# Performance work log

Measured on AMD Instinct MI355X. Metric: run time of the kernel, lower is better.

The kernel has to match this reference:

```python
import jax, jax.numpy as jnp
import numpy as np

N, E, D, H, G, L, EF = 50000, 800000, 128, 256, 512, 3, 8
BN_EPS = 1e-5


def _bn(h, g, b):
    # torch BatchNorm1d in training mode: biased batch stats over the node axis
    m = h.mean(0)
    v = h.var(0)
    return g * (h - m) * jax.lax.rsqrt(v + BN_EPS) + b


def setup_inputs() -> dict:
    ks = jax.random.split(jax.random.key(0), 12)
    sc = 0.05
    return {
        "x": jax.random.normal(ks[0], (N, D), jnp.float32),
        "edge_attr": jax.random.normal(ks[1], (E, EF), jnp.float32),
        "vn_emb": jnp.zeros((1, D), jnp.float32),  # init.constant_(0)
        "We": jax.random.normal(ks[2], (L, EF, D)) * sc,
        "be": jnp.zeros((L, D)),
        "W1": jax.random.normal(ks[3], (L, D, H)) * sc,
        "b1": jnp.zeros((L, H)),
        "g1": jnp.ones((L, H)),
        "bt1": jnp.zeros((L, H)),
        "W2": jax.random.normal(ks[4], (L, H, D)) * sc,
        "b2": jnp.zeros((L, D)),
        "gb": jnp.ones((L, D)),
        "bb": jnp.zeros((L, D)),
        "Wv1": jax.random.normal(ks[5], (L - 1, D, H)) * sc,
        "bv1": jnp.zeros((L - 1, H)),
        "gv1": jnp.ones((L - 1, H)),
        "btv1": jnp.zeros((L - 1, H)),
        "Wv2": jax.random.normal(ks[6], (L - 1, H, D)) * sc,
        "bv2": jnp.zeros((L - 1, D)),
        "gv2": jnp.ones((L - 1, D)),
        "btv2": jnp.zeros((L - 1, D)),
        "edge_index": jax.random.randint(ks[7], (2, E), 0, N),
        "batch": jnp.sort(jax.random.randint(ks[8], (N,), 0, G)),
    }


def reference(x, edge_attr, vn_emb, We, be, W1, b1, g1, bt1, W2, b2, gb, bb,
              Wv1, bv1, gv1, btv1, Wv2, bv2, gv2, btv2, edge_index, batch):
    src, dst = edge_index[0], edge_index[1]
    vn = jnp.broadcast_to(vn_emb, (G, D))  # Embedding(1, D) looked up for every graph
    h = x  # node_encoder is None -> encoded_node = x
    for l in range(L):
        h_in = h + vn[batch]                              # virtual-node broadcast (gather)
        e = edge_attr @ We[l] + be[l]                     # per-layer edge encoder
        msg = jax.nn.relu(h_in[src] + e)                  # GIN message, [E, D]
        aggr = jax.ops.segment_sum(msg, dst, num_segments=N)
        z = h_in + aggr                                   # (1+eps)*h + aggr, eps=0
        z = jax.nn.relu(_bn(z @ W1[l] + b1[l], g1[l], bt1[l]))
        h = _bn(z @ W2[l] + b2[l], gb[l], bb[l])          # conv MLP out + outer BatchNorm
        if l < L - 1:
            h = jax.nn.relu(h)                            # dropout ratio 0 -> identity
            pooled = jax.ops.segment_sum(h_in, batch, num_segments=G) + vn
            t = jax.nn.relu(_bn(pooled @ Wv1[l] + bv1[l], gv1[l], btv1[l]))
            vn = jax.nn.relu(_bn(t @ Wv2[l] + bv2[l], gv2[l], btv2[l]))
    return h  # JK == 'last'
```

## Files before the change

kernel.cpp:

```cpp
#include <hip/hip_runtime.h>
#include <hip/hip_bf16.h>

#define N_NODES 50000
#define N_EDGES 800000
#define DIM 128
#define HID 256
#define N_GRAPH 512
#define N_LAYER 3
#define EFEAT 8
#define BN_EPS 1e-5f
#define MAX_GROUPS 240000
#define AGGR_WAVES 8192

typedef unsigned short u16;
typedef unsigned int u32;

using bf16x8_t = short __attribute__((ext_vector_type(8)));
using f32x4_t  = float __attribute__((ext_vector_type(4)));
using f32x2    = float __attribute__((ext_vector_type(2)));
using f32x4v   = float __attribute__((ext_vector_type(4)));


__device__ __forceinline__ void atomic_add_f(float* p, float v) {
    unsafeAtomicAdd(p, v);
}
__device__ __forceinline__ u16 f2bf(float x) {
    union { float f; u32 u; } v; v.f = x;
    u32 r = v.u + 0x7FFF + ((v.u >> 16) & 1);
    return (u16)(r >> 16);
}
__device__ __forceinline__ float bf2f(u16 u) {
    union { u32 i; float f; } v; v.i = (u32)u << 16; return v.f;
}
__device__ __forceinline__ float2 up2(u32 p) {
    return make_float2(bf2f((u16)(p & 0xFFFF)), bf2f((u16)(p >> 16)));
}
__device__ __forceinline__ u32 pk2(float a, float b) {
    return (u32)f2bf(a) | ((u32)f2bf(b) << 16);
}
__device__ __forceinline__ f32x2 up2p(u32 p) {
    union { u32 u[2]; f32x2 f; } v;
    v.u[0] = p << 16;
    v.u[1] = p & 0xFFFF0000u;
    return v.f;
}
__device__ __forceinline__ f32x2 splat2(float x) {
    f32x2 r; r.x = x; r.y = x; return r;
}

__global__ __launch_bounds__(256) void wconv_kernel(
    const float* __restrict__ W1, const float* __restrict__ W2,
    u16* __restrict__ W1t, u16* __restrict__ W2t)
{
    int idx = blockIdx.x * 256 + threadIdx.x;
    if (idx >= 6 * 32768) return;
    int m = idx >> 15;
    int off = idx & 32767;
    int l = m >> 1;
    if ((m & 1) == 0) {
        int r = off >> 8, c = off & 255;
        W1t[(size_t)l * 32768 + c * 128 + r] = f2bf(W1[(size_t)l * 32768 + r * 256 + c]);
    } else {
        int r = off >> 7, c = off & 127;
        W2t[(size_t)l * 32768 + c * 256 + r] = f2bf(W2[(size_t)l * 32768 + r * 128 + c]);
    }
}

__global__ __launch_bounds__(256) void hist_rank_kernel(
    const int* __restrict__ ei, int* __restrict__ deg, int* __restrict__ rank)
{
    int e = blockIdx.x * 256 + threadIdx.x;
    if (e >= N_EDGES) return;
    int dst = ei[N_EDGES + e];
    rank[e] = atomicAdd(&deg[dst], 1);
}

__global__ __launch_bounds__(1024) void scan_kernel(const int* __restrict__ deg, int* __restrict__ grpptr) {
    __shared__ int wsum[16];
    __shared__ int carry;
    int tid = threadIdx.x;
    if (tid == 0) { carry = 0; grpptr[0] = 0; }
    __syncthreads();
    for (int base = 0; base < N_NODES; base += 1024) {
        int i = base + tid;
        int v = (i < N_NODES) ? ((deg[i] + 3) >> 2) : 0;
        int lane = tid & 63, w = tid >> 6;
        int s = v;
        #pragma unroll
        for (int d = 1; d < 64; d <<= 1) { int t = __shfl_up(s, d); if (lane >= d) s += t; }
        if (lane == 63) wsum[w] = s;
        __syncthreads();
        if (tid < 64) {
            int t = (tid < 16) ? wsum[tid] : 0;
            #pragma unroll
            for (int d = 1; d < 16; d <<= 1) { int u = __shfl_up(t, d); if (tid >= d) t += u; }
            if (tid < 16) wsum[tid] = t;
        }
        __syncthreads();
        int excl = (w > 0) ? wsum[w - 1] : 0;
        int incl = s + excl + carry;
        if (i < N_NODES) grpptr[i + 1] = incl;
        __syncthreads();
        if (tid == 0) carry += wsum[15];
        __syncthreads();
    }
}

__global__ __launch_bounds__(256) void padinit_kernel(uint4* __restrict__ rec4, int nslots) {
    int i = blockIdx.x * 256 + threadIdx.x;
    if (i >= nslots) return;
    int g = i / 9;
    int j = i - g * 9;
    uint4 v;
    if (j == 0) {
        u32 s = (u32)N_NODES << 8;
        v = make_uint4(s, s, s, s);
    } else {
        v = make_uint4(0u, 0u, 0u, 0u);
    }
    rec4[i] = v;
}

__global__ void negrow_kernel(u16* __restrict__ hin) {
    int l = threadIdx.x;
    *(u32*)(hin + (size_t)N_NODES * DIM + l * 2) = 0xFF7FFF7Fu;
}

__global__ __launch_bounds__(256) void scatter_kernel(
    const int* __restrict__ ei, const float* __restrict__ ea,
    const int* __restrict__ rank, const int* __restrict__ grpptr,
    char* __restrict__ rec)
{
    int e = blockIdx.x * 256 + threadIdx.x;
    if (e >= N_EDGES) return;
    int src = __builtin_nontemporal_load(ei + e);
    int dst = __builtin_nontemporal_load(ei + N_EDGES + e);
    int rk  = __builtin_nontemporal_load(rank + e);
    int grp = grpptr[dst] + (rk >> 2);
    int j = rk & 3;
    f32x4v lo = __builtin_nontemporal_load((const f32x4v*)(ea + (size_t)e * EFEAT));
    f32x4v hi = __builtin_nontemporal_load((const f32x4v*)(ea + (size_t)e * EFEAT + 4));
    char* rb = rec + (size_t)grp * 144;
    *(u32*)(rb + j * 4) = (u32)src << 8;
    *(f32x4v*)(rb + 16 + j * 32) = lo;
    *(f32x4v*)(rb + 32 + j * 32) = hi;
}

__global__ __launch_bounds__(256) void wstart_kernel(
    const int* __restrict__ grpptr, int* __restrict__ wstart)
{
    int w = blockIdx.x * 256 + threadIdx.x;
    if (w > AGGR_WAVES) return;
    if (w == AGGR_WAVES) { wstart[w] = N_NODES; return; }
    int Gt = grpptr[N_NODES];
    int q = (int)(((long long)w * Gt) / AGGR_WAVES);
    int lo = 0, hi = N_NODES;
    while (lo < hi) { int mid = (lo + hi) >> 1; if (grpptr[mid] < q) lo = mid + 1; else hi = mid; }
    wstart[w] = lo;
}

template <bool USEBN, int VNM>
__global__ __launch_bounds__(256) void hin_kernel(
    const float* __restrict__ src,
    const float* __restrict__ sum2, const float* __restrict__ ss2,
    const float* __restrict__ g, const float* __restrict__ b, float invN,
    const int* __restrict__ batch,
    const float* __restrict__ vn_emb,
    const float* __restrict__ vnpre, const float* __restrict__ vsum, const float* __restrict__ vss,
    const float* __restrict__ gv, const float* __restrict__ btv, float invG,
    u16* __restrict__ hin, int total4)
{
    int idx = blockIdx.x * 256 + threadIdx.x;
    if (idx >= total4) return;
    int base = idx * 4;
    int n = base >> 7;
    int c = base & (DIM - 1);
    float4 v = *(const float4*)(src + base);
    float o[4] = {v.x, v.y, v.z, v.w};
    if (USEBN) {
        #pragma unroll
        for (int j = 0; j < 4; ++j) {
            int cj = c + j;
            float m = sum2[cj] * invN;
            float var = ss2[cj] * invN - m * m;
            float r = rsqrtf(var + BN_EPS);
            float a = g[cj] * r;
            o[j] = fmaxf(fmaf(a, o[j], b[cj] - m * a), 0.f);
        }
    }
    int grp = batch[n];
    if (VNM == 0) {
        const float4 w = *(const float4*)(vn_emb + c);
        o[0] += w.x; o[1] += w.y; o[2] += w.z; o[3] += w.w;
    } else {
        const float4 vp = *(const float4*)(vnpre + (size_t)grp * DIM + c);
        float vv[4] = {vp.x, vp.y, vp.z, vp.w};
        #pragma unroll
        for (int j = 0; j < 4; ++j) {
            int cj = c + j;
            float m = vsum[cj] * invG;
            float var = vss[cj] * invG - m * m;
            float r = rsqrtf(var + BN_EPS);
            float a = gv[cj] * r;
            o[j] += fmaxf(fmaf(a, vv[j], btv[cj] - m * a), 0.f);
        }
    }
    uint2 pk;
    pk.x = pk2(o[0], o[1]);
    pk.y = pk2(o[2], o[3]);
    *(uint2*)(hin + base) = pk;
}

__device__ __forceinline__ void edge_term_f(
    u32 h, f32x4v ea, f32x4v eb, const f32x2* rW, f32x2 rB, f32x2& acc)
{
    f32x2 ex = rB;
    ex = __builtin_elementwise_fma(splat2(ea.x), rW[0], ex);
    ex = __builtin_elementwise_fma(splat2(ea.y), rW[1], ex);
    ex = __builtin_elementwise_fma(splat2(ea.z), rW[2], ex);
    ex = __builtin_elementwise_fma(splat2(ea.w), rW[3], ex);
    ex = __builtin_elementwise_fma(splat2(eb.x), rW[4], ex);
    ex = __builtin_elementwise_fma(splat2(eb.y), rW[5], ex);
    ex = __builtin_elementwise_fma(splat2(eb.z), rW[6], ex);
    ex = __builtin_elementwise_fma(splat2(eb.w), rW[7], ex);
    f32x2 s = up2p(h) + ex;
    s = __builtin_elementwise_max(s, splat2(0.f));
    acc += s;
}

__global__ __launch_bounds__(256) void aggr_kernel(
    const int* __restrict__ grpptr, const char* __restrict__ rec,
    const float* __restrict__ Wel, const float* __restrict__ bel,
    const u16* __restrict__ hin, u16* __restrict__ z,
    const int* __restrict__ wstart)
{
    const int lane = threadIdx.x & 63;
    const int cb = lane * 4;
    const int wid = __builtin_amdgcn_readfirstlane((blockIdx.x << 2) + (threadIdx.x >> 6));

    f32x2 rW[EFEAT];
    #pragma unroll
    for (int k = 0; k < EFEAT; ++k) {
        float2 t = *(const float2*)(Wel + k * DIM + lane * 2);
        rW[k].x = t.x; rW[k].y = t.y;
    }
    float2 tb = *(const float2*)(bel + lane * 2);
    f32x2 rB; rB.x = tb.x; rB.y = tb.y;

    const char* hinB = (const char*)hin;
    int n = wstart[wid];
    const int n1 = wstart[wid + 1];

    while (n < n1 && grpptr[n + 1] == grpptr[n]) {
        f32x2 a0 = up2p(*(const u32*)(hinB + ((u32)n << 8) + cb));
        *(u32*)(z + ((size_t)n << 7) + lane * 2) = pk2(a0.x, a0.y);
        ++n;
    }
    if (n < n1) {
        int g = grpptr[n];
        const int gTot = grpptr[n1];
        int gEnd = grpptr[n + 1];
        f32x2 acc = up2p(*(const u32*)(hinB + ((u32)n << 8) + cb));
        const char* rb = rec + (size_t)g * 144;

        uint4 so = *(const uint4*)rb;
        u32 h0 = *(const u32*)(hinB + so.x + cb);
        u32 h1 = *(const u32*)(hinB + so.y + cb);
        u32 h2 = *(const u32*)(hinB + so.z + cb);
        u32 h3 = *(const u32*)(hinB + so.w + cb);
        f32x4v e0a = *(const f32x4v*)(rb + 16);
        f32x4v e0b = *(const f32x4v*)(rb + 32);
        f32x4v e1a = *(const f32x4v*)(rb + 48);
        f32x4v e1b = *(const f32x4v*)(rb + 64);
        f32x4v e2a = *(const f32x4v*)(rb + 80);
        f32x4v e2b = *(const f32x4v*)(rb + 96);
        f32x4v e3a = *(const f32x4v*)(rb + 112);
        f32x4v e3b = *(const f32x4v*)(rb + 128);
        uint4 soN = *(const uint4*)(rb + 144);

        #pragma unroll 2
        for (; g < gTot; ++g, rb += 144) {
            u32 i0 = *(const u32*)(hinB + soN.x + cb);
            u32 i1 = *(const u32*)(hinB + soN.y + cb);
            u32 i2 = *(const u32*)(hinB + soN.z + cb);
            u32 i3 = *(const u32*)(hinB + soN.w + cb);
            f32x4v f0a = *(const f32x4v*)(rb + 160);
            f32x4v f0b = *(const f32x4v*)(rb + 176);
            f32x4v f1a = *(const f32x4v*)(rb + 192);
            f32x4v f1b = *(const f32x4v*)(rb + 208);
            f32x4v f2a = *(const f32x4v*)(rb + 224);
            f32x4v f2b = *(const f32x4v*)(rb + 240);
            f32x4v f3a = *(const f32x4v*)(rb + 256);
            f32x4v f3b = *(const f32x4v*)(rb + 272);
            uint4 soNN = *(const uint4*)(rb + 288);
            edge_term_f(h0, e0a, e0b, rW, rB, acc);
            edge_term_f(h1, e1a, e1b, rW, rB, acc);
            edge_term_f(h2, e2a, e2b, rW, rB, acc);
            edge_term_f(h3, e3a, e3b, rW, rB, acc);
            h0 = i0; h1 = i1; h2 = i2; h3 = i3;
            e0a = f0a; e0b = f0b; e1a = f1a; e1b = f1b;
            e2a = f2a; e2b = f2b; e3a = f3a; e3b = f3b;
            soN = soNN;
            if (g + 1 == gEnd) {
                *(u32*)(z + ((size_t)n << 7) + lane * 2) = pk2(acc.x, acc.y);
                ++n;
                if (g + 1 < gTot) {
                    while (grpptr[n + 1] == grpptr[n]) {
                        f32x2 a0 = up2p(*(const u32*)(hinB + ((u32)n << 8) + cb));
                        *(u32*)(z + ((size_t)n << 7) + lane * 2) = pk2(a0.x, a0.y);
                        ++n;
                    }
                    acc = up2p(*(const u32*)(hinB + ((u32)n << 8) + cb));
                    gEnd = grpptr[n + 1];
                }
            }
        }
    }
    while (n < n1) {
        f32x2 a0 = up2p(*(const u32*)(hinB + ((u32)n << 8) + cb));
        *(u32*)(z + ((size_t)n << 7) + lane * 2) = pk2(a0.x, a0.y);
        ++n;
    }
}

template <int MODE, bool CBF16>
__global__ __launch_bounds__(256) void gemm_bf16_kernel(
    const u16* __restrict__ Aa,
    const float* __restrict__ sSum, const float* __restrict__ sSS,
    const float* __restrict__ gA, const float* __restrict__ btA, float invCnt,
    const u16* __restrict__ Bt,
    const float* __restrict__ bias,
    void* __restrict__ CoutV,
    float* __restrict__ outSum, float* __restrict__ outSS,
    int M, int K, int Nc)
{
    constexpr int BM = 128, BN = 128, BK = 128;
    constexpr int LDA = BK + 8;
    __shared__ u16 As[BM * LDA];
    __shared__ u16 Bs[64 * LDA];
    __shared__ float csum[BN], css[BN];

    const int tid = threadIdx.x;
    const int wave = tid >> 6, lane = tid & 63;
    const int row0 = blockIdx.x * BM, col0 = blockIdx.y * BN;
    const int w_m = (wave & 1) * 64, w_n = (wave >> 1) * 32;
    const int quad = lane >> 4, l16 = lane & 15;

    if (tid < BN) { csum[tid] = 0.f; css[tid] = 0.f; }

    f32x4_t acc[4][4];
    #pragma unroll
    for (int mi = 0; mi < 4; ++mi)
        #pragma unroll
        for (int ni = 0; ni < 4; ++ni)
            acc[mi][ni] = (f32x4_t){0.f, 0.f, 0.f, 0.f};

    const int kc = (tid & 15) * 8;
    const int nkt = K / BK;

    for (int kt = 0; kt < nkt; ++kt) {
        float af[8], bf_[8];
        if (MODE == 1) {
            #pragma unroll
            for (int j = 0; j < 8; ++j) {
                int kg = kt * BK + kc + j;
                float m = sSum[kg] * invCnt;
                float var = sSS[kg] * invCnt - m * m;
                float r = rsqrtf(var + BN_EPS);
                float a = gA[kg] * r;
                af[j] = a;
                bf_[j] = btA[kg] - m * a;
            }
        }
        #pragma unroll
        for (int it = 0; it < 8; ++it) {
            int chunk = it * 256 + tid;
            int row = chunk >> 4;
            int gr = row0 + row; if (gr >= M) gr = M - 1;
            uint4 q = *(const uint4*)(Aa + (size_t)gr * K + kt * BK + kc);
            if (MODE == 1) {
                float2 p0 = up2(q.x), p1 = up2(q.y), p2 = up2(q.z), p3 = up2(q.w);
                p0.x = fmaxf(fmaf(af[0], p0.x, bf_[0]), 0.f);
                p0.y = fmaxf(fmaf(af[1], p0.y, bf_[1]), 0.f);
                p1.x = fmaxf(fmaf(af[2], p1.x, bf_[2]), 0.f);
                p1.y = fmaxf(fmaf(af[3], p1.y, bf_[3]), 0.f);
                p2.x = fmaxf(fmaf(af[4], p2.x, bf_[4]), 0.f);
                p2.y = fmaxf(fmaf(af[5], p2.y, bf_[5]), 0.f);
                p3.x = fmaxf(fmaf(af[6], p3.x, bf_[6]), 0.f);
                p3.y = fmaxf(fmaf(af[7], p3.y, bf_[7]), 0.f);
                q.x = pk2(p0.x, p0.y); q.y = pk2(p1.x, p1.y);
                q.z = pk2(p2.x, p2.y); q.w = pk2(p3.x, p3.y);
            }
            *(uint4*)(As + row * LDA + kc) = q;
        }
        #pragma unroll
        for (int half = 0; half < 2; ++half) {
            #pragma unroll
            for (int it = 0; it < 4; ++it) {
                int chunk = it * 256 + tid;
                int n = chunk >> 4;
                uint4 q = *(const uint4*)(Bt + (size_t)(col0 + half * 64 + n) * K + kt * BK + kc);
                *(uint4*)(Bs + n * LDA + kc) = q;
            }
            __syncthreads();
            #pragma unroll
            for (int ks = 0; ks < 4; ++ks) {
                bf16x8_t a_frag[4], b_frag[2];
                #pragma unroll
                for (int mi = 0; mi < 4; ++mi)
                    a_frag[mi] = *(const bf16x8_t*)(As + (w_m + mi * 16 + l16) * LDA + ks * 32 + quad * 8);
                #pragma unroll
                for (int ni = 0; ni < 2; ++ni)
                    b_frag[ni] = *(const bf16x8_t*)(Bs + (w_n + ni * 16 + l16) * LDA + ks * 32 + quad * 8);
                #pragma unroll
                for (int mi = 0; mi < 4; ++mi)
                    #pragma unroll
                    for (int ni = 0; ni < 2; ++ni)
                        acc[mi][half * 2 + ni] = __builtin_amdgcn_mfma_f32_16x16x32_bf16(
                            a_frag[mi], b_frag[ni], acc[mi][half * 2 + ni], 0, 0, 0);
            }
            __syncthreads();
        }
    }

    u16* Cb = (u16*)CoutV;
    float* Cf = (float*)CoutV;
    #pragma unroll
    for (int half = 0; half < 2; ++half)
    #pragma unroll
    for (int ni = 0; ni < 2; ++ni) {
        int ccol = half * 64 + w_n + ni * 16 + l16;
        int col = col0 + ccol;
        float bv = bias[col];
        float s = 0.f, qs = 0.f;
        #pragma unroll
        for (int mi = 0; mi < 4; ++mi) {
            int rbase = row0 + w_m + mi * 16 + quad * 4;
            #pragma unroll
            for (int reg = 0; reg < 4; ++reg) {
                int gr = rbase + reg;
                if (gr < M) {
                    float o = acc[mi][half * 2 + ni][reg] + bv;
                    s += o;
                    qs += o * o;
                    if (CBF16) Cb[(size_t)gr * Nc + col] = f2bf(o);
                    else       Cf[(size_t)gr * Nc + col] = o;
                }
            }
        }
        s += __shfl_xor(s, 16);  s += __shfl_xor(s, 32);
        qs += __shfl_xor(qs, 16);  qs += __shfl_xor(qs, 32);
        if (quad == 0) {
            atomicAdd(&csum[ccol], s);
            atomicAdd(&css[ccol], qs);
        }
    }
    __syncthreads();
    if (tid < BN) {
        atomic_add_f(outSum + col0 + tid, csum[tid]);
        atomic_add_f(outSS + col0 + tid, css[tid]);
    }
}

template <int MODE>
__global__ __launch_bounds__(256) void gemm_kernel(
    const float* __restrict__ Aa,
    const float* __restrict__ sSum, const float* __restrict__ sSS,
    const float* __restrict__ gA, const float* __restrict__ btA, float invCnt,
    const float* __restrict__ B, const float* __restrict__ bias,
    float* __restrict__ Cout, float* __restrict__ outSum, float* __restrict__ outSS,
    int M, int K, int Nc)
{
    __shared__ float As[16][68];
    __shared__ float Bs[16][64];
    __shared__ float alphaS[256], betaS[256];
    __shared__ float csum[64], css[64];

    const int tid = threadIdx.x;
    const int tx = tid & 15, ty = tid >> 4;
    const int row0 = blockIdx.x * 64, col0 = blockIdx.y * 64;

    if (tid < 64) { csum[tid] = 0.f; css[tid] = 0.f; }
    if (MODE == 1) {
        for (int k = tid; k < K; k += 256) {
            float m = sSum[k] * invCnt;
            float var = sSS[k] * invCnt - m * m;
            float r = rsqrtf(var + BN_EPS);
            float a = gA[k] * r;
            alphaS[k] = a;
            betaS[k] = btA[k] - m * a;
        }
    }
    __syncthreads();

    float acc[4][4];
    #pragma unroll
    for (int i = 0; i < 4; ++i)
        #pragma unroll
        for (int j = 0; j < 4; ++j) acc[i][j] = 0.f;

    const int lr = tid >> 2;
    const int lk = (tid & 3) * 4;
    const int bk = tid >> 4;
    const int bc = tx * 4;

    for (int kt = 0; kt < K; kt += 16) {
        int gr = row0 + lr;
        float4 va = make_float4(0.f, 0.f, 0.f, 0.f);
        if (gr < M) {
            va = *(const float4*)(Aa + (size_t)gr * K + kt + lk);
            if (MODE == 1) {
                int k0 = kt + lk;
                va.x = fmaxf(fmaf(alphaS[k0 + 0], va.x, betaS[k0 + 0]), 0.f);
                va.y = fmaxf(fmaf(alphaS[k0 + 1], va.y, betaS[k0 + 1]), 0.f);
                va.z = fmaxf(fmaf(alphaS[k0 + 2], va.z, betaS[k0 + 2]), 0.f);
                va.w = fmaxf(fmaf(alphaS[k0 + 3], va.w, betaS[k0 + 3]), 0.f);
            }
        }
        As[lk + 0][lr] = va.x;
        As[lk + 1][lr] = va.y;
        As[lk + 2][lr] = va.z;
        As[lk + 3][lr] = va.w;
        const float4 vb4 = *(const float4*)(B + (size_t)(kt + bk) * Nc + col0 + bc);
        *(float4*)&Bs[bk][bc] = vb4;
        __syncthreads();
        #pragma unroll
        for (int kk = 0; kk < 16; ++kk) {
            const float4 a4 = *(const float4*)&As[kk][ty * 4];
            const float4 b4 = *(const float4*)&Bs[kk][tx * 4];
            float av[4] = {a4.x, a4.y, a4.z, a4.w};
            float bv4[4] = {b4.x, b4.y, b4.z, b4.w};
            #pragma unroll
            for (int i = 0; i < 4; ++i)
                #pragma unroll
                for (int j = 0; j < 4; ++j)
                    acc[i][j] = fmaf(av[i], bv4[j], acc[i][j]);
        }
        __syncthreads();
    }

    const float4 bvv = *(const float4*)(bias + col0 + tx * 4);
    float bias4[4] = {bvv.x, bvv.y, bvv.z, bvv.w};
    float ps[4] = {0.f, 0.f, 0.f, 0.f};
    float pq[4] = {0.f, 0.f, 0.f, 0.f};
    #pragma unroll
    for (int i = 0; i < 4; ++i) {
        int gr = row0 + ty * 4 + i;
        if (gr < M) {
            float o[4];
            #pragma unroll
            for (int j = 0; j < 4; ++j) {
                o[j] = acc[i][j] + bias4[j];
                ps[j] += o[j];
                pq[j] += o[j] * o[j];
            }
            *(float4*)(Cout + (size_t)gr * Nc + col0 + tx * 4) = make_float4(o[0], o[1], o[2], o[3]);
        }
    }
    #pragma unroll
    for (int j = 0; j < 4; ++j) {
        atomicAdd(&csum[tx * 4 + j], ps[j]);
        atomicAdd(&css[tx * 4 + j], pq[j]);
    }
    __syncthreads();
    if (tid < 64) {
        atomic_add_f(outSum + col0 + tid, csum[tid]);
        atomic_add_f(outSS + col0 + tid, css[tid]);
    }
}

template <int VNM>
__global__ __launch_bounds__(128) void pooled_seg_kernel(
    const u16* __restrict__ hin, const int* __restrict__ batch,
    const float* __restrict__ vn_emb,
    const float* __restrict__ vnpre, const float* __restrict__ vsum, const float* __restrict__ vss,
    const float* __restrict__ gv, const float* __restrict__ btv, float invG,
    float* __restrict__ pooled)
{
    int g = blockIdx.x;
    int c = threadIdx.x;
    int lo = 0, hi = N_NODES;
    while (lo < hi) { int mid = (lo + hi) >> 1; if (batch[mid] < g) lo = mid + 1; else hi = mid; }
    int start = lo;
    hi = N_NODES;
    while (lo < hi) { int mid = (lo + hi) >> 1; if (batch[mid] < g + 1) lo = mid + 1; else hi = mid; }
    int end = lo;
    float acc;
    if (VNM == 0) {
        acc = vn_emb[c];
    } else {
        float m = vsum[c] * invG;
        float var = vss[c] * invG - m * m;
        float r = rsqrtf(var + BN_EPS);
        float a = gv[c] * r;
        acc = fmaxf(fmaf(a, vnpre[(size_t)g * DIM + c], btv[c] - m * a), 0.f);
    }
    float a0 = 0.f, a1 = 0.f, a2 = 0.f, a3 = 0.f;
    int n = start;
    for (; n + 3 < end; n += 4) {
        a0 += bf2f(hin[(size_t)(n + 0) * DIM + c]);
        a1 += bf2f(hin[(size_t)(n + 1) * DIM + c]);
        a2 += bf2f(hin[(size_t)(n + 2) * DIM + c]);
        a3 += bf2f(hin[(size_t)(n + 3) * DIM + c]);
    }
    for (; n < end; ++n) a0 += bf2f(hin[(size_t)n * DIM + c]);
    acc += (a0 + a1) + (a2 + a3);
    pooled[(size_t)g * DIM + c] = acc;
}

__global__ __launch_bounds__(256) void final_bn_kernel(
    float* __restrict__ outp, const float* __restrict__ sum2, const float* __restrict__ ss2,
    const float* __restrict__ g, const float* __restrict__ b, float invN, int total4)
{
    int idx = blockIdx.x * 256 + threadIdx.x;
    if (idx >= total4) return;
    int base = idx * 4;
    int c = base & (DIM - 1);
    float4 v = *(const float4*)(outp + base);
    float o[4] = {v.x, v.y, v.z, v.w};
    #pragma unroll
    for (int j = 0; j < 4; ++j) {
        int cj = c + j;
        float m = sum2[cj] * invN;
        float var = ss2[cj] * invN - m * m;
        float r = rsqrtf(var + BN_EPS);
        float a = g[cj] * r;
        o[j] = fmaf(a, o[j], b[cj] - m * a);
    }
    *(float4*)(outp + base) = make_float4(o[0], o[1], o[2], o[3]);
}

extern "C" void kernel_launch(void* const* d_in, const int* in_sizes, int n_in,
                              void* d_out, int out_size, void* d_ws, size_t ws_size,
                              hipStream_t stream) {
    const float* x         = (const float*)d_in[0];
    const float* edge_attr = (const float*)d_in[1];
    const float* vn_emb    = (const float*)d_in[2];
    const float* We        = (const float*)d_in[3];
    const float* be        = (const float*)d_in[4];
    const float* W1        = (const float*)d_in[5];
    const float* b1        = (const float*)d_in[6];
    const float* g1v       = (const float*)d_in[7];
    const float* bt1       = (const float*)d_in[8];
    const float* W2        = (const float*)d_in[9];
    const float* b2        = (const float*)d_in[10];
    const float* gb        = (const float*)d_in[11];
    const float* bb        = (const float*)d_in[12];
    const float* Wv1       = (const float*)d_in[13];
    const float* bv1       = (const float*)d_in[14];
    const float* gv1       = (const float*)d_in[15];
    const float* btv1      = (const float*)d_in[16];
    const float* Wv2       = (const float*)d_in[17];
    const float* bv2       = (const float*)d_in[18];
    const float* gv2       = (const float*)d_in[19];
    const float* btv2      = (const float*)d_in[20];
    const int* edge_index  = (const int*)d_in[21];
    const int* batch       = (const int*)d_in[22];
    float* outp = (float*)d_out;

    auto au = [](size_t x) { return (x + 255) & ~(size_t)255; };
    char* p = (char*)d_ws;
    u16* h_in   = (u16*)p;  p += au((size_t)(N_NODES + 1) * DIM * 2);
    u16* z_bf   = (u16*)p;  p += au((size_t)N_NODES * DIM * 2);
    u16* c1_bf  = (u16*)p;  p += au((size_t)N_NODES * HID * 2);
    u16* W1t    = (u16*)p;  p += au((size_t)3 * 32768 * 2);
    u16* W2t    = (u16*)p;  p += au((size_t)3 * 32768 * 2);
    float* pooled = (float*)p;  p += au((size_t)N_GRAPH * DIM * 4);
    float* tpre   = (float*)p;  p += au((size_t)N_GRAPH * HID * 4);
    float* vnpre  = (float*)p;  p += au((size_t)N_GRAPH * DIM * 4);
    float* stats  = (float*)p;  p += au(2048 * 4);
    float* sum1 = stats,        *ss1 = stats + 256;
    float* sum2 = stats + 512,  *ss2 = stats + 640;
    float* vsum1 = stats + 768, *vss1 = stats + 1024;
    float* vsum2 = stats + 1280, *vss2 = stats + 1408;
    int* grpptr = (int*)p;  p += au((size_t)(N_NODES + 1) * 4);
    int* wstart = (int*)p;  p += au((size_t)(AGGR_WAVES + 1) * 4);
    char* rec   = p;        p += au((size_t)(MAX_GROUPS + 4) * 144);
    int* deg  = (int*)z_bf;
    int* rank = (int*)c1_bf;

    const float invN = 1.0f / (float)N_NODES;
    const float invG = 1.0f / (float)N_GRAPH;
    const int total4 = N_NODES * DIM / 4;

    hipMemsetAsync(deg, 0, N_NODES * sizeof(int), stream);
    hist_rank_kernel<<<(N_EDGES + 255) / 256, 256, 0, stream>>>(edge_index, deg, rank);
    scan_kernel<<<1, 1024, 0, stream>>>(deg, grpptr);
    {
        int nslots = (MAX_GROUPS + 4) * 9;
        padinit_kernel<<<(nslots + 255) / 256, 256, 0, stream>>>((uint4*)rec, nslots);
    }
    negrow_kernel<<<1, 64, 0, stream>>>(h_in);
    scatter_kernel<<<(N_EDGES + 255) / 256, 256, 0, stream>>>(
        edge_index, edge_attr, rank, grpptr, rec);
    wstart_kernel<<<(AGGR_WAVES + 256) / 256, 256, 0, stream>>>(grpptr, wstart);
    wconv_kernel<<<768, 256, 0, stream>>>(W1, W2, W1t, W2t);

    const int AGGR_BLOCKS = AGGR_WAVES / 4;

    for (int l = 0; l < N_LAYER; ++l) {
        if (l == 0)
            hin_kernel<false, 0><<<(total4 + 255) / 256, 256, 0, stream>>>(
                x, nullptr, nullptr, nullptr, nullptr, 0.f, batch,
                vn_emb, nullptr, nullptr, nullptr, nullptr, nullptr, 0.f,
                h_in, total4);
        else
            hin_kernel<true, 1><<<(total4 + 255) / 256, 256, 0, stream>>>(
                outp, sum2, ss2, gb + (size_t)(l - 1) * DIM, bb + (size_t)(l - 1) * DIM, invN, batch,
                nullptr, vnpre, vsum2, vss2,
                gv2 + (size_t)(l - 1) * DIM, btv2 + (size_t)(l - 1) * DIM, invG,
                h_in, total4);

        if (l == 0)
            pooled_seg_kernel<0><<<N_GRAPH, 128, 0, stream>>>(
                h_in, batch, vn_emb, nullptr, nullptr, nullptr, nullptr, nullptr, 0.f, pooled);
        else if (l < N_LAYER - 1)
            pooled_seg_kernel<1><<<N_GRAPH, 128, 0, stream>>>(
                h_in, batch, nullptr, vnpre, vsum2, vss2,
                gv2 + (size_t)(l - 1) * DIM, btv2 + (size_t)(l - 1) * DIM, invG, pooled);

        hipMemsetAsync(stats, 0, 2048 * sizeof(float), stream);

        aggr_kernel<<<AGGR_BLOCKS, 256, 0, stream>>>(
            grpptr, rec, We + (size_t)l * EFEAT * DIM, be + (size_t)l * DIM,
            h_in, z_bf, wstart);

        dim3 g1d((N_NODES + 127) / 128, HID / 128);
        gemm_bf16_kernel<0, true><<<g1d, 256, 0, stream>>>(
            z_bf, nullptr, nullptr, nullptr, nullptr, 0.f,
            W1t + (size_t)l * 32768, b1 + (size_t)l * HID,
            (void*)c1_bf, sum1, ss1, N_NODES, DIM, HID);

        dim3 g2d((N_NODES + 127) / 128, DIM / 128);
        gemm_bf16_kernel<1, false><<<g2d, 256, 0, stream>>>(
            c1_bf, sum1, ss1, g1v + (size_t)l * HID, bt1 + (size_t)l * HID, invN,
            W2t + (size_t)l * 32768, b2 + (size_t)l * DIM,
            (void*)outp, sum2, ss2, N_NODES, HID, DIM);

        if (l < N_LAYER - 1) {
            dim3 g3d(N_GRAPH / 64, HID / 64);
            gemm_kernel<0><<<g3d, 256, 0, stream>>>(
                pooled, nullptr, nullptr, nullptr, nullptr, 0.f,
                Wv1 + (size_t)l * DIM * HID, bv1 + (size_t)l * HID,
                tpre, vsum1, vss1, N_GRAPH, DIM, HID);

            dim3 g4d(N_GRAPH / 64, DIM / 64);
            gemm_kernel<1><<<g4d, 256, 0, stream>>>(
                tpre, vsum1, vss1, gv1 + (size_t)l * HID, btv1 + (size_t)l * HID, invG,
                Wv2 + (size_t)l * HID * DIM, bv2 + (size_t)l * DIM,
                vnpre, vsum2, vss2, N_GRAPH, HID, DIM);
        }
    }

    final_bn_kernel<<<(total4 + 255) / 256, 256, 0, stream>>>(
        outp, sum2, ss2, gb + (size_t)2 * DIM, bb + (size_t)2 * DIM, invN, total4);
}
```

Measured before the change: 786.1 us.

## Store edge indices in CSR records and gather edge_attr directly in aggregation

The per-group edge record shrinks from 144 bytes, which held copies of the edge features, to 32 bytes holding only a source offset and an edge offset per edge. The aggregation kernel now gathers the 8 edge features straight from edge_attr through those offsets. This cuts the scatter kernel's write traffic and the padinit work, at the cost of an extra indirect, less contiguous read of edge_attr in every layer. The pooled segment-sum kernel is also changed to use 64 threads, each handling two channels with 32-bit bf16x2 loads.

```diff
diff --git a/kernel.cpp b/kernel.cpp
--- a/kernel.cpp
+++ b/kernel.cpp
@@ -109,16 +109,8 @@
 __global__ __launch_bounds__(256) void padinit_kernel(uint4* __restrict__ rec4, int nslots) {
     int i = blockIdx.x * 256 + threadIdx.x;
     if (i >= nslots) return;
-    int g = i / 9;
-    int j = i - g * 9;
-    uint4 v;
-    if (j == 0) {
-        u32 s = (u32)N_NODES << 8;
-        v = make_uint4(s, s, s, s);
-    } else {
-        v = make_uint4(0u, 0u, 0u, 0u);
-    }
-    rec4[i] = v;
+    u32 s = (u32)N_NODES << 8;
+    rec4[i] = make_uint4(s, 0u, s, 0u);
 }
 
 __global__ void negrow_kernel(u16* __restrict__ hin) {
@@ -127,7 +119,7 @@
 }
 
 __global__ __launch_bounds__(256) void scatter_kernel(
-    const int* __restrict__ ei, const float* __restrict__ ea,
+    const int* __restrict__ ei,
     const int* __restrict__ rank, const int* __restrict__ grpptr,
     char* __restrict__ rec)
 {
@@ -138,12 +130,10 @@
     int rk  = __builtin_nontemporal_load(rank + e);
     int grp = grpptr[dst] + (rk >> 2);
     int j = rk & 3;
-    f32x4v lo = __builtin_nontemporal_load((const f32x4v*)(ea + (size_t)e * EFEAT));
-    f32x4v hi = __builtin_nontemporal_load((const f32x4v*)(ea + (size_t)e * EFEAT + 4));
-    char* rb = rec + (size_t)grp * 144;
-    *(u32*)(rb + j * 4) = (u32)src << 8;
-    *(f32x4v*)(rb + 16 + j * 32) = lo;
-    *(f32x4v*)(rb + 32 + j * 32) = hi;
+    uint2 v;
+    v.x = (u32)src << 8;
+    v.y = (u32)e << 5;
+    *(uint2*)(rec + (size_t)grp * 32 + j * 8) = v;
 }
 
 __global__ __launch_bounds__(256) void wstart_kernel(
@@ -230,6 +220,7 @@
 
 __global__ __launch_bounds__(256) void aggr_kernel(
     const int* __restrict__ grpptr, const char* __restrict__ rec,
+    const float* __restrict__ eaF,
     const float* __restrict__ Wel, const float* __restrict__ bel,
     const u16* __restrict__ hin, u16* __restrict__ z,
     const int* __restrict__ wstart)
@@ -248,6 +239,7 @@
     f32x2 rB; rB.x = tb.x; rB.y = tb.y;
 
     const char* hinB = (const char*)hin;
+    const char* eaB = (const char*)eaF;
     int n = wstart[wid];
     const int n1 = wstart[wid + 1];
 
@@ -261,46 +253,49 @@
         const int gTot = grpptr[n1];
         int gEnd = grpptr[n + 1];
         f32x2 acc = up2p(*(const u32*)(hinB + ((u32)n << 8) + cb));
-        const char* rb = rec + (size_t)g * 144;
-
-        uint4 so = *(const uint4*)rb;
-        u32 h0 = *(const u32*)(hinB + so.x + cb);
-        u32 h1 = *(const u32*)(hinB + so.y + cb);
-        u32 h2 = *(const u32*)(hinB + so.z + cb);
-        u32 h3 = *(const u32*)(hinB + so.w + cb);
-        f32x4v e0a = *(const f32x4v*)(rb + 16);
-        f32x4v e0b = *(const f32x4v*)(rb + 32);
-        f32x4v e1a = *(const f32x4v*)(rb + 48);
-        f32x4v e1b = *(const f32x4v*)(rb + 64);
-        f32x4v e2a = *(const f32x4v*)(rb + 80);
-        f32x4v e2b = *(const f32x4v*)(rb + 96);
-        f32x4v e3a = *(const f32x4v*)(rb + 112);
-        f32x4v e3b = *(const f32x4v*)(rb + 128);
-        uint4 soN = *(const uint4*)(rb + 144);
+        const char* rb = rec + (size_t)g * 32;
+
+        uint4 r0 = *(const uint4*)rb;
+        uint4 r1 = *(const uint4*)(rb + 16);
+        u32 h0 = *(const u32*)(hinB + r0.x + cb);
+        u32 h1 = *(const u32*)(hinB + r0.z + cb);
+        u32 h2 = *(const u32*)(hinB + r1.x + cb);
+        u32 h3 = *(const u32*)(hinB + r1.z + cb);
+        f32x4v A0a = *(const f32x4v*)(eaB + r0.y);
+        f32x4v A0b = *(const f32x4v*)(eaB + r0.y + 16);
+        f32x4v A1a = *(const f32x4v*)(eaB + r0.w);
+        f32x4v A1b = *(const f32x4v*)(eaB + r0.w + 16);
+        f32x4v A2a = *(const f32x4v*)(eaB + r1.y);
+        f32x4v A2b = *(const f32x4v*)(eaB + r1.y + 16);
+        f32x4v A3a = *(const f32x4v*)(eaB + r1.w);
+        f32x4v A3b = *(const f32x4v*)(eaB + r1.w + 16);
+        uint4 r0N = *(const uint4*)(rb + 32);
+        uint4 r1N = *(const uint4*)(rb + 48);
 
         #pragma unroll 2
-        for (; g < gTot; ++g, rb += 144) {
-            u32 i0 = *(const u32*)(hinB + soN.x + cb);
-            u32 i1 = *(const u32*)(hinB + soN.y + cb);
-            u32 i2 = *(const u32*)(hinB + soN.z + cb);
-            u32 i3 = *(const u32*)(hinB + soN.w + cb);
-            f32x4v f0a = *(const f32x4v*)(rb + 160);
-            f32x4v f0b = *(const f32x4v*)(rb + 176);
-            f32x4v f1a = *(const f32x4v*)(rb + 192);
-            f32x4v f1b = *(const f32x4v*)(rb + 208);
-            f32x4v f2a = *(const f32x4v*)(rb + 224);
-            f32x4v f2b = *(const f32x4v*)(rb + 240);
-            f32x4v f3a = *(const f32x4v*)(rb + 256);
-            f32x4v f3b = *(const f32x4v*)(rb + 272);
-            uint4 soNN = *(const uint4*)(rb + 288);
-            edge_term_f(h0, e0a, e0b, rW, rB, acc);
-            edge_term_f(h1, e1a, e1b, rW, rB, acc);
-            edge_term_f(h2, e2a, e2b, rW, rB, acc);
-            edge_term_f(h3, e3a, e3b, rW, rB, acc);
+        for (; g < gTot; ++g, rb += 32) {
+            u32 i0 = *(const u32*)(hinB + r0N.x + cb);
+            u32 i1 = *(const u32*)(hinB + r0N.z + cb);
+            u32 i2 = *(const u32*)(hinB + r1N.x + cb);
+            u32 i3 = *(const u32*)(hinB + r1N.z + cb);
+            f32x4v B0a = *(const f32x4v*)(eaB + r0N.y);
+            f32x4v B0b = *(const f32x4v*)(eaB + r0N.y + 16);
+            f32x4v B1a = *(const f32x4v*)(eaB + r0N.w);
+            f32x4v B1b = *(const f32x4v*)(eaB + r0N.w + 16);
+            f32x4v B2a = *(const f32x4v*)(eaB + r1N.y);
+            f32x4v B2b = *(const f32x4v*)(eaB + r1N.y + 16);
+            f32x4v B3a = *(const f32x4v*)(eaB + r1N.w);
+            f32x4v B3b = *(const f32x4v*)(eaB + r1N.w + 16);
+            uint4 r0NN = *(const uint4*)(rb + 64);
+            uint4 r1NN = *(const uint4*)(rb + 80);
+            edge_term_f(h0, A0a, A0b, rW, rB, acc);
+            edge_term_f(h1, A1a, A1b, rW, rB, acc);
+            edge_term_f(h2, A2a, A2b, rW, rB, acc);
+            edge_term_f(h3, A3a, A3b, rW, rB, acc);
             h0 = i0; h1 = i1; h2 = i2; h3 = i3;
-            e0a = f0a; e0b = f0b; e1a = f1a; e1b = f1b;
-            e2a = f2a; e2b = f2b; e3a = f3a; e3b = f3b;
-            soN = soNN;
+            A0a = B0a; A0b = B0b; A1a = B1a; A1b = B1b;
+            A2a = B2a; A2b = B2b; A3a = B3a; A3b = B3b;
+            r0N = r0NN; r1N = r1NN;
             if (g + 1 == gEnd) {
                 *(u32*)(z + ((size_t)n << 7) + lane * 2) = pk2(acc.x, acc.y);
                 ++n;
@@ -570,7 +565,7 @@
 }
 
 template <int VNM>
-__global__ __launch_bounds__(128) void pooled_seg_kernel(
+__global__ __launch_bounds__(64) void pooled_seg_kernel(
     const u16* __restrict__ hin, const int* __restrict__ batch,
     const float* __restrict__ vn_emb,
     const float* __restrict__ vnpre, const float* __restrict__ vsum, const float* __restrict__ vss,
@@ -578,34 +573,45 @@
     float* __restrict__ pooled)
 {
     int g = blockIdx.x;
-    int c = threadIdx.x;
+    int lane = threadIdx.x;
+    int c2 = lane * 2;
     int lo = 0, hi = N_NODES;
     while (lo < hi) { int mid = (lo + hi) >> 1; if (batch[mid] < g) lo = mid + 1; else hi = mid; }
     int start = lo;
     hi = N_NODES;
     while (lo < hi) { int mid = (lo + hi) >> 1; if (batch[mid] < g + 1) lo = mid + 1; else hi = mid; }
     int end = lo;
-    float acc;
+
+    f32x2 acc;
     if (VNM == 0) {
-        acc = vn_emb[c];
+        float2 w = *(const float2*)(vn_emb + c2);
+        acc.x = w.x; acc.y = w.y;
     } else {
-        float m = vsum[c] * invG;
-        float var = vss[c] * invG - m * m;
-        float r = rsqrtf(var + BN_EPS);
-        float a = gv[c] * r;
-        acc = fmaxf(fmaf(a, vnpre[(size_t)g * DIM + c], btv[c] - m * a), 0.f);
-    }
-    float a0 = 0.f, a1 = 0.f, a2 = 0.f, a3 = 0.f;
+        float2 vs = *(const float2*)(vsum + c2);
+        float2 vq = *(const float2*)(vss + c2);
+        float2 gg = *(const float2*)(gv + c2);
+        float2 bt = *(const float2*)(btv + c2);
+        float2 vp = *(const float2*)(vnpre + (size_t)g * DIM + c2);
+        float m0 = vs.x * invG, m1 = vs.y * invG;
+        float va0 = vq.x * invG - m0 * m0, va1 = vq.y * invG - m1 * m1;
+        float a0 = gg.x * rsqrtf(va0 + BN_EPS), a1 = gg.y * rsqrtf(va1 + BN_EPS);
+        acc.x = fmaxf(fmaf(a0, vp.x, bt.x - m0 * a0), 0.f);
+        acc.y = fmaxf(fmaf(a1, vp.y, bt.y - m1 * a1), 0.f);
+    }
+
+    const char* hinB = (const char*)hin;
+    const int cb = lane * 4;
+    f32x2 s0 = splat2(0.f), s1 = splat2(0.f), s2 = splat2(0.f), s3 = splat2(0.f);
     int n = start;
     for (; n + 3 < end; n += 4) {
-        a0 += bf2f(hin[(size_t)(n + 0) * DIM + c]);
-        a1 += bf2f(hin[(size_t)(n + 1) * DIM + c]);
-        a2 += bf2f(hin[(size_t)(n + 2) * DIM + c]);
-        a3 += bf2f(hin[(size_t)(n + 3) * DIM + c]);
-    }
-    for (; n < end; ++n) a0 += bf2f(hin[(size_t)n * DIM + c]);
-    acc += (a0 + a1) + (a2 + a3);
-    pooled[(size_t)g * DIM + c] = acc;
+        s0 += up2p(*(const u32*)(hinB + ((size_t)(n + 0) << 8) + cb));
+        s1 += up2p(*(const u32*)(hinB + ((size_t)(n + 1) << 8) + cb));
+        s2 += up2p(*(const u32*)(hinB + ((size_t)(n + 2) << 8) + cb));
+        s3 += up2p(*(const u32*)(hinB + ((size_t)(n + 3) << 8) + cb));
+    }
+    for (; n < end; ++n) s0 += up2p(*(const u32*)(hinB + ((size_t)n << 8) + cb));
+    acc += (s0 + s1) + (s2 + s3);
+    *(float2*)(pooled + (size_t)g * DIM + c2) = make_float2(acc.x, acc.y);
 }
 
 __global__ __launch_bounds__(256) void final_bn_kernel(
@@ -675,7 +681,7 @@
     float* vsum2 = stats + 1280, *vss2 = stats + 1408;
     int* grpptr = (int*)p;  p += au((size_t)(N_NODES + 1) * 4);
     int* wstart = (int*)p;  p += au((size_t)(AGGR_WAVES + 1) * 4);
-    char* rec   = p;        p += au((size_t)(MAX_GROUPS + 4) * 144);
+    char* rec   = p;        p += au((size_t)(MAX_GROUPS + 4) * 32 + 256);
     int* deg  = (int*)z_bf;
     int* rank = (int*)c1_bf;
 
@@ -687,12 +693,12 @@
     hist_rank_kernel<<<(N_EDGES + 255) / 256, 256, 0, stream>>>(edge_index, deg, rank);
     scan_kernel<<<1, 1024, 0, stream>>>(deg, grpptr);
     {
-        int nslots = (MAX_GROUPS + 4) * 9;
+        int nslots = (MAX_GROUPS + 4) * 2;
         padinit_kernel<<<(nslots + 255) / 256, 256, 0, stream>>>((uint4*)rec, nslots);
     }
     negrow_kernel<<<1, 64, 0, stream>>>(h_in);
     scatter_kernel<<<(N_EDGES + 255) / 256, 256, 0, stream>>>(
-        edge_index, edge_attr, rank, grpptr, rec);
+        edge_index, rank, grpptr, rec);
     wstart_kernel<<<(AGGR_WAVES + 256) / 256, 256, 0, stream>>>(grpptr, wstart);
     wconv_kernel<<<768, 256, 0, stream>>>(W1, W2, W1t, W2t);
 
@@ -712,17 +718,17 @@
                 h_in, total4);
 
         if (l == 0)
-            pooled_seg_kernel<0><<<N_GRAPH, 128, 0, stream>>>(
+            pooled_seg_kernel<0><<<N_GRAPH, 64, 0, stream>>>(
                 h_in, batch, vn_emb, nullptr, nullptr, nullptr, nullptr, nullptr, 0.f, pooled);
         else if (l < N_LAYER - 1)
-            pooled_seg_kernel<1><<<N_GRAPH, 128, 0, stream>>>(
+            pooled_seg_kernel<1><<<N_GRAPH, 64, 0, stream>>>(
                 h_in, batch, nullptr, vnpre, vsum2, vss2,
                 gv2 + (size_t)(l - 1) * DIM, btv2 + (size_t)(l - 1) * DIM, invG, pooled);
 
         hipMemsetAsync(stats, 0, 2048 * sizeof(float), stream);
 
         aggr_kernel<<<AGGR_BLOCKS, 256, 0, stream>>>(
-            grpptr, rec, We + (size_t)l * EFEAT * DIM, be + (size_t)l * DIM,
+            grpptr, rec, edge_attr, We + (size_t)l * EFEAT * DIM, be + (size_t)l * DIM,
             h_in, z_bf, wstart);
 
         dim3 g1d((N_NODES + 127) / 128, HID / 128);
```

Result: faster. 768.2 us (-2.3%).

## Split edge record build into compact scatter plus coalesced expand pass

Applied to the files above, without the earlier changes.

The scatter kernel now writes a compact 8-byte (src, edge-offset) record per padded slot. A new expand kernel walks the slots in order, gathers the edge attributes and writes the 144-byte group records sequentially, which replaces 32-byte random scatter writes with coalesced writes but adds random reads of edge_attr and an extra launch. Padding init now covers only the compact array; padded slots point at the sentinel node and edge offset 0. The pooled segment-sum kernel is also changed to 64 threads, each loading two bf16 channels per node.

```diff
diff --git a/kernel.cpp b/kernel.cpp
--- a/kernel.cpp
+++ b/kernel.cpp
@@ -106,19 +106,11 @@
     }
 }
 
-__global__ __launch_bounds__(256) void padinit_kernel(uint4* __restrict__ rec4, int nslots) {
+__global__ __launch_bounds__(256) void padinit_kernel(uint4* __restrict__ rec4, int nq) {
     int i = blockIdx.x * 256 + threadIdx.x;
-    if (i >= nslots) return;
-    int g = i / 9;
-    int j = i - g * 9;
-    uint4 v;
-    if (j == 0) {
-        u32 s = (u32)N_NODES << 8;
-        v = make_uint4(s, s, s, s);
-    } else {
-        v = make_uint4(0u, 0u, 0u, 0u);
-    }
-    rec4[i] = v;
+    if (i >= nq) return;
+    u32 s = (u32)N_NODES << 8;
+    rec4[i] = make_uint4(s, 0u, s, 0u);
 }
 
 __global__ void negrow_kernel(u16* __restrict__ hin) {
@@ -127,21 +119,37 @@
 }
 
 __global__ __launch_bounds__(256) void scatter_kernel(
-    const int* __restrict__ ei, const float* __restrict__ ea,
+    const int* __restrict__ ei,
     const int* __restrict__ rank, const int* __restrict__ grpptr,
-    char* __restrict__ rec)
+    uint2* __restrict__ srec)
 {
     int e = blockIdx.x * 256 + threadIdx.x;
     if (e >= N_EDGES) return;
     int src = __builtin_nontemporal_load(ei + e);
     int dst = __builtin_nontemporal_load(ei + N_EDGES + e);
     int rk  = __builtin_nontemporal_load(rank + e);
-    int grp = grpptr[dst] + (rk >> 2);
-    int j = rk & 3;
-    f32x4v lo = __builtin_nontemporal_load((const f32x4v*)(ea + (size_t)e * EFEAT));
-    f32x4v hi = __builtin_nontemporal_load((const f32x4v*)(ea + (size_t)e * EFEAT + 4));
-    char* rb = rec + (size_t)grp * 144;
-    *(u32*)(rb + j * 4) = (u32)src << 8;
+    int slot = grpptr[dst] * 4 + rk;
+    slot = (grpptr[dst] + (rk >> 2)) * 4 + (rk & 3);
+    uint2 v;
+    v.x = (u32)src << 8;
+    v.y = (u32)e << 5;
+    srec[slot] = v;
+}
+
+__global__ __launch_bounds__(256) void expand_kernel(
+    const uint2* __restrict__ srec, const float* __restrict__ ea,
+    char* __restrict__ brec, int nslots)
+{
+    int i = blockIdx.x * 256 + threadIdx.x;
+    if (i >= nslots) return;
+    int g = i >> 2;
+    int j = i & 3;
+    uint2 v = srec[i];
+    const char* eaB = (const char*)ea;
+    f32x4v lo = *(const f32x4v*)(eaB + v.y);
+    f32x4v hi = *(const f32x4v*)(eaB + v.y + 16);
+    char* rb = brec + (size_t)g * 144;
+    *(u32*)(rb + j * 4) = v.x;
     *(f32x4v*)(rb + 16 + j * 32) = lo;
     *(f32x4v*)(rb + 32 + j * 32) = hi;
 }
@@ -570,7 +578,7 @@
 }
 
 template <int VNM>
-__global__ __launch_bounds__(128) void pooled_seg_kernel(
+__global__ __launch_bounds__(64) void pooled_seg_kernel(
     const u16* __restrict__ hin, const int* __restrict__ batch,
     const float* __restrict__ vn_emb,
     const float* __restrict__ vnpre, const float* __restrict__ vsum, const float* __restrict__ vss,
@@ -578,34 +586,45 @@
     float* __restrict__ pooled)
 {
     int g = blockIdx.x;
-    int c = threadIdx.x;
+    int lane = threadIdx.x;
+    int c2 = lane * 2;
     int lo = 0, hi = N_NODES;
     while (lo < hi) { int mid = (lo + hi) >> 1; if (batch[mid] < g) lo = mid + 1; else hi = mid; }
     int start = lo;
     hi = N_NODES;
     while (lo < hi) { int mid = (lo + hi) >> 1; if (batch[mid] < g + 1) lo = mid + 1; else hi = mid; }
     int end = lo;
-    float acc;
+
+    f32x2 acc;
     if (VNM == 0) {
-        acc = vn_emb[c];
+        float2 w = *(const float2*)(vn_emb + c2);
+        acc.x = w.x; acc.y = w.y;
     } else {
-        float m = vsum[c] * invG;
-        float var = vss[c] * invG - m * m;
-        float r = rsqrtf(var + BN_EPS);
-        float a = gv[c] * r;
-        acc = fmaxf(fmaf(a, vnpre[(size_t)g * DIM + c], btv[c] - m * a), 0.f);
-    }
-    float a0 = 0.f, a1 = 0.f, a2 = 0.f, a3 = 0.f;
+        float2 vs = *(const float2*)(vsum + c2);
+        float2 vq = *(const float2*)(vss + c2);
+        float2 gg = *(const float2*)(gv + c2);
+        float2 bt = *(const float2*)(btv + c2);
+        float2 vp = *(const float2*)(vnpre + (size_t)g * DIM + c2);
+        float m0 = vs.x * invG, m1 = vs.y * invG;
+        float va0 = vq.x * invG - m0 * m0, va1 = vq.y * invG - m1 * m1;
+        float a0 = gg.x * rsqrtf(va0 + BN_EPS), a1 = gg.y * rsqrtf(va1 + BN_EPS);
+        acc.x = fmaxf(fmaf(a0, vp.x, bt.x - m0 * a0), 0.f);
+        acc.y = fmaxf(fmaf(a1, vp.y, bt.y - m1 * a1), 0.f);
+    }
+
+    const char* hinB = (const char*)hin;
+    const int cb = lane * 4;
+    f32x2 s0 = splat2(0.f), s1 = splat2(0.f), s2 = splat2(0.f), s3 = splat2(0.f);
     int n = start;
     for (; n + 3 < end; n += 4) {
-        a0 += bf2f(hin[(size_t)(n + 0) * DIM + c]);
-        a1 += bf2f(hin[(size_t)(n + 1) * DIM + c]);
-        a2 += bf2f(hin[(size_t)(n + 2) * DIM + c]);
-        a3 += bf2f(hin[(size_t)(n + 3) * DIM + c]);
-    }
-    for (; n < end; ++n) a0 += bf2f(hin[(size_t)n * DIM + c]);
-    acc += (a0 + a1) + (a2 + a3);
-    pooled[(size_t)g * DIM + c] = acc;
+        s0 += up2p(*(const u32*)(hinB + ((size_t)(n + 0) << 8) + cb));
+        s1 += up2p(*(const u32*)(hinB + ((size_t)(n + 1) << 8) + cb));
+        s2 += up2p(*(const u32*)(hinB + ((size_t)(n + 2) << 8) + cb));
+        s3 += up2p(*(const u32*)(hinB + ((size_t)(n + 3) << 8) + cb));
+    }
+    for (; n < end; ++n) s0 += up2p(*(const u32*)(hinB + ((size_t)n << 8) + cb));
+    acc += (s0 + s1) + (s2 + s3);
+    *(float2*)(pooled + (size_t)g * DIM + c2) = make_float2(acc.x, acc.y);
 }
 
 __global__ __launch_bounds__(256) void final_bn_kernel(
@@ -675,24 +694,25 @@
     float* vsum2 = stats + 1280, *vss2 = stats + 1408;
     int* grpptr = (int*)p;  p += au((size_t)(N_NODES + 1) * 4);
     int* wstart = (int*)p;  p += au((size_t)(AGGR_WAVES + 1) * 4);
-    char* rec   = p;        p += au((size_t)(MAX_GROUPS + 4) * 144);
-    int* deg  = (int*)z_bf;
-    int* rank = (int*)c1_bf;
+    char* brec  = p;        p += au((size_t)(MAX_GROUPS + 4) * 144 + 512);
+    int* deg   = (int*)z_bf;
+    int* rank  = (int*)c1_bf;
+    uint2* srec = (uint2*)(c1_bf + au((size_t)N_EDGES * 4) / 2);
 
     const float invN = 1.0f / (float)N_NODES;
     const float invG = 1.0f / (float)N_GRAPH;
     const int total4 = N_NODES * DIM / 4;
+    const int nslots = (MAX_GROUPS + 4) * 4;
 
     hipMemsetAsync(deg, 0, N_NODES * sizeof(int), stream);
     hist_rank_kernel<<<(N_EDGES + 255) / 256, 256, 0, stream>>>(edge_index, deg, rank);
     scan_kernel<<<1, 1024, 0, stream>>>(deg, grpptr);
-    {
-        int nslots = (MAX_GROUPS + 4) * 9;
-        padinit_kernel<<<(nslots + 255) / 256, 256, 0, stream>>>((uint4*)rec, nslots);
-    }
+    padinit_kernel<<<(nslots / 2 + 255) / 256, 256, 0, stream>>>((uint4*)srec, nslots / 2);
     negrow_kernel<<<1, 64, 0, stream>>>(h_in);
     scatter_kernel<<<(N_EDGES + 255) / 256, 256, 0, stream>>>(
-        edge_index, edge_attr, rank, grpptr, rec);
+        edge_index, rank, grpptr, srec);
+    expand_kernel<<<(nslots + 255) / 256, 256, 0, stream>>>(
+        srec, edge_attr, brec, nslots);
     wstart_kernel<<<(AGGR_WAVES + 256) / 256, 256, 0, stream>>>(grpptr, wstart);
     wconv_kernel<<<768, 256, 0, stream>>>(W1, W2, W1t, W2t);
 
@@ -712,17 +732,17 @@
                 h_in, total4);
 
         if (l == 0)
-            pooled_seg_kernel<0><<<N_GRAPH, 128, 0, stream>>>(
+            pooled_seg_kernel<0><<<N_GRAPH, 64, 0, stream>>>(
                 h_in, batch, vn_emb, nullptr, nullptr, nullptr, nullptr, nullptr, 0.f, pooled);
         else if (l < N_LAYER - 1)
-            pooled_seg_kernel<1><<<N_GRAPH, 128, 0, stream>>>(
+            pooled_seg_kernel<1><<<N_GRAPH, 64, 0, stream>>>(
                 h_in, batch, nullptr, vnpre, vsum2, vss2,
                 gv2 + (size_t)(l - 1) * DIM, btv2 + (size_t)(l - 1) * DIM, invG, pooled);
 
         hipMemsetAsync(stats, 0, 2048 * sizeof(float), stream);
 
         aggr_kernel<<<AGGR_BLOCKS, 256, 0, stream>>>(
-            grpptr, rec, We + (size_t)l * EFEAT * DIM, be + (size_t)l * DIM,
+            grpptr, brec, We + (size_t)l * EFEAT * DIM, be + (size_t)l * DIM,
             h_in, z_bf, wstart);
 
         dim3 g1d((N_NODES + 127) / 128, HID / 128);
```

Result: no change. 779.1 us (-0.9%).
